# Kernel tuning notes

Measured on AMD Instinct MI355X. Metric: run time of the kernel, lower is better.

Reference implementation:

```python
import jax, jax.numpy as jnp
import numpy as np

DIM, SSM, RNN = 1024, 64, 128


def setup_inputs() -> dict:
    key = jax.random.key(0)
    ks = jax.random.split(key, 16)
    s = 0.02
    B, N = 8, 2048
    return {
        'x': jax.random.normal(ks[0], (B, N, DIM), jnp.float32),
        'A': jax.random.normal(ks[1], (SSM, SSM), jnp.float32) * s,
        'Bw': jax.random.normal(ks[2], (SSM, DIM), jnp.float32) * s,
        'Bb': jnp.zeros((SSM,), jnp.float32),
        'Cw': jax.random.normal(ks[3], (DIM, SSM), jnp.float32) * s,
        'Cb': jnp.zeros((DIM,), jnp.float32),
        'Dw': jax.random.normal(ks[4], (DIM, DIM), jnp.float32) * s,
        'Db': jnp.zeros((DIM,), jnp.float32),
        'W_ih': jax.random.normal(ks[5], (3 * RNN, DIM), jnp.float32) * s,
        'b_ih': jnp.zeros((3 * RNN,), jnp.float32),
        'W_hh': jax.random.normal(ks[6], (3 * RNN, RNN), jnp.float32) * s,
        'b_hh': jnp.zeros((3 * RNN,), jnp.float32),
        'proj_w': jax.random.normal(ks[7], (DIM, RNN), jnp.float32) * s,
        'proj_b': jnp.zeros((DIM,), jnp.float32),
        'gate_w': jax.random.normal(ks[8], (2, DIM), jnp.float32) * s,
        'gate_b': jnp.zeros((2,), jnp.float32),
    }


def reference(x, A, Bw, Bb, Cw, Cb, Dw, Db, W_ih, b_ih, W_hh, b_hh, proj_w, proj_b, gate_w, gate_b):
    B, N, D = x.shape
    R = W_hh.shape[1]
    # Precompute all input-side projections once (time-parallel GEMMs).
    bx = jnp.einsum('bnd,sd->bns', x, Bw) + Bb            # [B,N,SSM]
    dx = jnp.einsum('bnd,ed->bne', x, Dw) + Db            # [B,N,D]
    gx = jax.nn.sigmoid(jnp.einsum('bnd,gd->bng', x, gate_w) + gate_b)  # [B,N,2]
    ih = jnp.einsum('bnd,rd->bnr', x, W_ih) + b_ih        # [B,N,3R]
    # time-major for scan
    bx_t = jnp.swapaxes(bx, 0, 1)
    dx_t = jnp.swapaxes(dx, 0, 1)
    gx_t = jnp.swapaxes(gx, 0, 1)
    ih_t = jnp.swapaxes(ih, 0, 1)

    h_ssm0 = jnp.zeros((B, A.shape[0]), x.dtype)
    h_rnn0 = jnp.zeros((B, R), x.dtype)

    def step(carry, inp):
        h_ssm, h_rnn = carry
        bxt, dxt, gxt, iht = inp
        h_ssm = jax.nn.silu(h_ssm @ A.T + bxt)
        y_ssm = h_ssm @ Cw.T + Cb + dxt
        # GRUCell (torch semantics)
        hh = h_rnn @ W_hh.T + b_hh
        i_r, i_z, i_n = jnp.split(iht, 3, axis=-1)
        h_r, h_z, h_n = jnp.split(hh, 3, axis=-1)
        r = jax.nn.sigmoid(i_r + h_r)
        z = jax.nn.sigmoid(i_z + h_z)
        n = jnp.tanh(i_n + r * h_n)
        h_rnn = (1.0 - z) * n + z * h_rnn
        y_rnn = h_rnn @ proj_w.T + proj_b
        fused = gxt[:, :1] * y_ssm + gxt[:, 1:2] * y_rnn
        return (h_ssm, h_rnn), fused

    _, out = jax.lax.scan(step, (h_ssm0, h_rnn0), (bx_t, dx_t, gx_t, ih_t))
    return jnp.swapaxes(out, 0, 1)  # [B,N,D]
```

## Files before the change

kernel.cpp:

```cpp
#include <hip/hip_runtime.h>


#define MROWS 16384
#define SEQ   2048
#define CH    16
#define NCH   (SEQ / CH)

typedef __attribute__((ext_vector_type(8))) short bf16x8;
typedef __attribute__((ext_vector_type(4))) float f32x4;

__device__ __forceinline__ float bf2f(unsigned short u) {
    union { unsigned int i; float f; } c; c.i = ((unsigned int)u) << 16; return c.f;
}
__device__ __forceinline__ unsigned short f2bf(float f) {
    union { float f; unsigned int i; } c; c.f = f;
    unsigned int x = c.i;
    return (unsigned short)((x + 0x7fffu + ((x >> 16) & 1u)) >> 16);
}
__device__ __forceinline__ unsigned int f2bf_pk(float lo, float hi) {
    unsigned int r;
    asm("v_cvt_pk_bf16_f32 %0, %1, %2" : "=v"(r) : "v"(lo), "v"(hi));
    return r;
}
__device__ __forceinline__ float ldin(const void* p, size_t i, int isf32) {
    return isf32 ? ((const float*)p)[i] : bf2f(((const unsigned short*)p)[i]);
}
__device__ __forceinline__ float sigf(float v) { return 1.f / (1.f + __expf(-v)); }
__device__ __forceinline__ float tanhf_fast(float v) { return 2.f * sigf(2.f * v) - 1.f; }

__global__ void sniff_kernel(const unsigned short* __restrict__ x, int* __restrict__ flag) {
    int tid = threadIdx.x;
    int big = 0;
    for (int i = tid; i < 1024; i += 64) {
        unsigned int e = (x[i] >> 7) & 0xFFu;
        big += (e >= 0xC0u) ? 1 : 0;
    }
#pragma unroll
    for (int off = 32; off; off >>= 1) big += __shfl_down(big, off);
    if (tid == 0) { flag[0] = (big >= 4) ? 1 : 0; flag[1] = 0; }
}

__global__ void zero_out_kernel(float* __restrict__ out) {
    size_t i = ((size_t)blockIdx.x * 256 + threadIdx.x) * 16;
#pragma unroll
    for (int u = 0; u < 16; u++) out[i + u] = 0.f;
}

__device__ __forceinline__ void cvt16(const void* src, unsigned short* dst,
                                      size_t i0, int isf32) {
#pragma unroll
    for (int q = 0; q < 2; q++) {
        size_t i = i0 + q * 8;
        if (isf32) {
            const float* s = (const float*)src + i;
            float4 a = *reinterpret_cast<const float4*>(s);
            float4 b = *reinterpret_cast<const float4*>(s + 4);
            union { bf16x8 v; unsigned int u[4]; } u;
            u.u[0] = f2bf_pk(a.x, a.y); u.u[1] = f2bf_pk(a.z, a.w);
            u.u[2] = f2bf_pk(b.x, b.y); u.u[3] = f2bf_pk(b.z, b.w);
            *reinterpret_cast<bf16x8*>(dst + i) = u.v;
        } else {
            *reinterpret_cast<bf16x8*>(dst + i) =
                *reinterpret_cast<const bf16x8*>((const unsigned short*)src + i);
        }
    }
}

__global__ __launch_bounds__(256) void cvt_x_kernel(
    const void* __restrict__ x, unsigned short* __restrict__ xb,
    const int* __restrict__ flagp) {
    int isf32 = *flagp;
    size_t i0 = ((size_t)blockIdx.x * 256 + threadIdx.x) * 16;
    cvt16(x, xb, i0, isf32);
}

__global__ __launch_bounds__(256) void cvt_w_kernel(
    const void* __restrict__ Dw,  const void* __restrict__ Wih,
    const void* __restrict__ pw,  const void* __restrict__ Cw,
    const void* __restrict__ Bw,  const void* __restrict__ bih,
    const void* __restrict__ Bb,  const void* __restrict__ Cb,
    const void* __restrict__ Db,  const void* __restrict__ pb,
    unsigned short* __restrict__ Dwb,  unsigned short* __restrict__ Wihb,
    unsigned short* __restrict__ pwb,  unsigned short* __restrict__ Cwb,
    unsigned short* __restrict__ Bwb,  unsigned short* __restrict__ bihb,
    unsigned short* __restrict__ Bbb,  unsigned short* __restrict__ Cbb,
    unsigned short* __restrict__ Dbb,  unsigned short* __restrict__ pbb,
    const int* __restrict__ flagp) {
    int isf32 = *flagp;
    int blk = blockIdx.x, tid = threadIdx.x;
    const void* src; unsigned short* dst; size_t base;
    if (blk < 256)      { src = Dw;  dst = Dwb;  base = (size_t)blk * 4096; }
    else if (blk < 352) { src = Wih; dst = Wihb; base = (size_t)(blk - 256) * 4096; }
    else if (blk < 384) { src = pw;  dst = pwb;  base = (size_t)(blk - 352) * 4096; }
    else if (blk < 400) { src = Cw;  dst = Cwb;  base = (size_t)(blk - 384) * 4096; }
    else if (blk < 416) { src = Bw;  dst = Bwb;  base = (size_t)(blk - 400) * 4096; }
    else {
        for (int i = tid; i < 384; i += 256) bihb[i] = f2bf(ldin(bih, i, isf32));
        if (tid < 64) Bbb[tid] = f2bf(ldin(Bb, tid, isf32));
        for (int i = tid; i < 1024; i += 256) {
            Cbb[i] = f2bf(ldin(Cb, i, isf32));
            Dbb[i] = f2bf(ldin(Db, i, isf32));
            pbb[i] = f2bf(ldin(pb, i, isf32));
        }
        return;
    }
    cvt16(src, dst, base + (size_t)tid * 16, isf32);
}

__device__ __forceinline__ void stage_tile(const void* __restrict__ g,
                                           int ld, int row0, int rowmax, int kb,
                                           short (*lds)[40], int tid, int isf32) {
#pragma unroll
    for (int q = 0; q < 2; q++) {
        int oct = q * 256 + tid;
        int row = oct >> 2, c8 = (oct & 3) << 3;
        int gr = row0 + row; if (gr > rowmax) gr = rowmax;
        size_t base = (size_t)gr * ld + kb + c8;
        bf16x8 v;
        if (isf32) {
            const float* gp = (const float*)g + base;
            float4 f0 = *reinterpret_cast<const float4*>(gp);
            float4 f1 = *reinterpret_cast<const float4*>(gp + 4);
            union { bf16x8 v8; unsigned int u[4]; } u;
            u.u[0] = f2bf_pk(f0.x, f0.y);
            u.u[1] = f2bf_pk(f0.z, f0.w);
            u.u[2] = f2bf_pk(f1.x, f1.y);
            u.u[3] = f2bf_pk(f1.z, f1.w);
            v = u.v8;
        } else {
            v = *reinterpret_cast<const bf16x8*>((const unsigned short*)g + base);
        }
        *reinterpret_cast<bf16x8*>(&lds[row][c8]) = v;
    }
}

__device__ __forceinline__ void mfma_tiles(const short (*As)[40], const short (*Bs)[40],
                                           int wm, int wn, int lane, f32x4 (*acc)[4]) {
    bf16x8 af[4], bfr[4];
    int m = lane & 15, ko = (lane >> 4) << 3;
#pragma unroll
    for (int i = 0; i < 4; i++)
        af[i] = *reinterpret_cast<const bf16x8*>(&As[wm + i * 16 + m][ko]);
#pragma unroll
    for (int j = 0; j < 4; j++)
        bfr[j] = *reinterpret_cast<const bf16x8*>(&Bs[wn + j * 16 + m][ko]);
#pragma unroll
    for (int i = 0; i < 4; i++)
#pragma unroll
        for (int j = 0; j < 4; j++)
            acc[i][j] = __builtin_amdgcn_mfma_f32_16x16x32_bf16(af[i], bfr[j], acc[i][j], 0, 0, 0);
}

__global__ __launch_bounds__(256) void gemm_bt_kernel(
    const void* __restrict__ A, const void* __restrict__ W,
    const void* __restrict__ bias, unsigned short* __restrict__ C,
    int M, int N, int K, const int* __restrict__ flagp) {
    __shared__ __align__(16) short As[128][40];
    __shared__ __align__(16) short Bs[128][40];
    int isf32 = *flagp;
    int tid = threadIdx.x, lane = tid & 63, wave = tid >> 6;
    int wm = (wave >> 1) << 6, wn = (wave & 1) << 6;
    int tileM = blockIdx.x << 7, tileN = blockIdx.y << 7;
    f32x4 acc[4][4];
    f32x4 z = {0.f, 0.f, 0.f, 0.f};
#pragma unroll
    for (int i = 0; i < 4; i++)
#pragma unroll
        for (int j = 0; j < 4; j++) acc[i][j] = z;

    for (int kb = 0; kb < K; kb += 32) {
        __syncthreads();
        stage_tile(A, K, tileM, M - 1, kb, As, tid, isf32);
        stage_tile(W, K, tileN, N - 1, kb, Bs, tid, isf32);
        __syncthreads();
        mfma_tiles(As, Bs, wm, wn, lane, acc);
    }
#pragma unroll
    for (int i = 0; i < 4; i++) {
#pragma unroll
        for (int j = 0; j < 4; j++) {
            int col = tileN + wn + j * 16 + (lane & 15);
            if (col < N) {
                float bv = ldin(bias, col, isf32);
                int row0 = tileM + wm + i * 16 + ((lane >> 4) << 2);
                unsigned int pk0 = f2bf_pk(acc[i][j][0] + bv, acc[i][j][1] + bv);
                unsigned int pk1 = f2bf_pk(acc[i][j][2] + bv, acc[i][j][3] + bv);
                C[(size_t)(row0 + 0) * N + col] = (unsigned short)(pk0 & 0xFFFFu);
                C[(size_t)(row0 + 1) * N + col] = (unsigned short)(pk0 >> 16);
                C[(size_t)(row0 + 2) * N + col] = (unsigned short)(pk1 & 0xFFFFu);
                C[(size_t)(row0 + 3) * N + col] = (unsigned short)(pk1 >> 16);
            }
        }
    }
}

__global__ __launch_bounds__(256) void gate_kernel(
    const void* __restrict__ x, const void* __restrict__ gw,
    const void* __restrict__ gb, float* __restrict__ gx, const int* __restrict__ flagp) {
    int isf32 = *flagp;
    int row = (blockIdx.x << 2) + (threadIdx.x >> 6);
    int lane = threadIdx.x & 63;
    size_t xoff = (size_t)row * 1024 + lane * 16;
    float a0 = 0.f, a1 = 0.f;
#pragma unroll
    for (int q = 0; q < 2; q++) {
#pragma unroll
        for (int e = 0; e < 8; e++) {
            size_t k = q * 8 + e;
            float xf = ldin(x, xoff + k, isf32);
            a0 += xf * ldin(gw, (size_t)lane * 16 + k, isf32);
            a1 += xf * ldin(gw, 1024 + (size_t)lane * 16 + k, isf32);
        }
    }
#pragma unroll
    for (int off = 32; off > 0; off >>= 1) {
        a0 += __shfl_down(a0, off);
        a1 += __shfl_down(a1, off);
    }
    if (lane == 0) {
        gx[row * 2]     = sigf(a0 + ldin(gb, 0, isf32));
        gx[row * 2 + 1] = sigf(a1 + ldin(gb, 1, isf32));
    }
}

__global__ __launch_bounds__(512) void scan_kernel(
    const void* __restrict__ Amat,
    const void* __restrict__ Whh,
    const void* __restrict__ bhh,
    const unsigned short* __restrict__ bxw,
    const unsigned short* __restrict__ ihw,
    unsigned short* __restrict__ hsw,
    unsigned short* __restrict__ hrw,
    const int* __restrict__ flagp) {
    int isf32 = *flagp;
    int b = blockIdx.x & 7;
    size_t rowbase = (size_t)b * SEQ;
    f32x4 zf = {0.f, 0.f, 0.f, 0.f};

    if (blockIdx.x < 8) {
        __shared__ __align__(16) unsigned short H[2][128];
        __shared__ __align__(16) unsigned short IH[2][CH][384];
        int tid = threadIdx.x, lane = tid & 63, w = tid >> 6;
        int col = lane & 15, quad = lane >> 4;
        int o = w * 16 + col;
        if (tid < 256) ((unsigned short*)H)[tid] = 0;
        bf16x8 Bf[3][4];
#pragma unroll
        for (int g = 0; g < 3; g++) {
            int n = g * 128 + o;
#pragma unroll
            for (int c = 0; c < 4; c++) {
                int k0 = c * 32 + quad * 8;
                bf16x8 v;
#pragma unroll
                for (int e = 0; e < 8; e++)
                    v[e] = (short)f2bf(ldin(Whh, (size_t)n * 128 + k0 + e, isf32));
                Bf[g][c] = v;
            }
        }
        float bias_r = ldin(bhh, o, isf32);
        float bias_z = ldin(bhh, 128 + o, isf32);
        float bias_n = ldin(bhh, 256 + o, isf32);
        float hprev = 0.f;
        bool gl = (quad == 0);
        const unsigned short* ihbase = ihw + rowbase * 384;
        bf16x8 stg0, stg1;
        stg0 = *reinterpret_cast<const bf16x8*>(ihbase + (size_t)tid * 8);
        if (tid < 256) stg1 = *reinterpret_cast<const bf16x8*>(ihbase + (size_t)(512 + tid) * 8);
        *reinterpret_cast<bf16x8*>(&IH[0][0][0] + (size_t)tid * 8) = stg0;
        if (tid < 256) *reinterpret_cast<bf16x8*>(&IH[0][0][0] + (size_t)(512 + tid) * 8) = stg1;
        stg0 = *reinterpret_cast<const bf16x8*>(ihbase + (size_t)CH * 384 + (size_t)tid * 8);
        if (tid < 256) stg1 = *reinterpret_cast<const bf16x8*>(ihbase + (size_t)CH * 384 + (size_t)(512 + tid) * 8);
        __syncthreads();

        int p = 0;
        for (int c = 0; c < NCH; c++) {
            int cur = c & 1;
            for (int tt = 0; tt < CH; tt++) {
                int t = c * CH + tt;
                bf16x8 Af[4];
#pragma unroll
                for (int cc = 0; cc < 4; cc++)
                    Af[cc] = *reinterpret_cast<const bf16x8*>(&H[p][cc * 32 + quad * 8]);
                float ir  = bf2f(IH[cur][tt][o]);
                float iz  = bf2f(IH[cur][tt][128 + o]);
                float inn = bf2f(IH[cur][tt][256 + o]);
                f32x4 accL[3], accH[3];
#pragma unroll
                for (int g = 0; g < 3; g++) { accL[g] = zf; accH[g] = zf; }
                __builtin_amdgcn_s_setprio(1);
#pragma unroll
                for (int g = 0; g < 3; g++) {
                    accL[g] = __builtin_amdgcn_mfma_f32_16x16x32_bf16(Af[0], Bf[g][0], accL[g], 0, 0, 0);
                    accH[g] = __builtin_amdgcn_mfma_f32_16x16x32_bf16(Af[2], Bf[g][2], accH[g], 0, 0, 0);
                    accL[g] = __builtin_amdgcn_mfma_f32_16x16x32_bf16(Af[1], Bf[g][1], accL[g], 0, 0, 0);
                    accH[g] = __builtin_amdgcn_mfma_f32_16x16x32_bf16(Af[3], Bf[g][3], accH[g], 0, 0, 0);
                }
                __builtin_amdgcn_s_setprio(0);
                if (tt == 8) {
                    if (c + 1 < NCH) {
                        unsigned short* dst = &IH[(c + 1) & 1][0][0];
                        *reinterpret_cast<bf16x8*>(dst + (size_t)tid * 8) = stg0;
                        if (tid < 256) *reinterpret_cast<bf16x8*>(dst + (size_t)(512 + tid) * 8) = stg1;
                    }
                    if (c + 2 < NCH) {
                        const unsigned short* src = ihbase + (size_t)(c + 2) * CH * 384;
                        stg0 = *reinterpret_cast<const bf16x8*>(src + (size_t)tid * 8);
                        if (tid < 256) stg1 = *reinterpret_cast<const bf16x8*>(src + (size_t)(512 + tid) * 8);
                    }
                }
                float sr = accL[0][0] + accH[0][0];
                float sz = accL[1][0] + accH[1][0];
                float sn = accL[2][0] + accH[2][0];
                float r  = sigf(ir + sr + bias_r);
                float zg = sigf(iz + sz + bias_z);
                float n  = tanhf_fast(inn + r * (sn + bias_n));
                float hnew = (1.f - zg) * n + zg * hprev;
                hprev = hnew;
                if (gl) {
                    unsigned short hb = f2bf(hnew);
                    H[p ^ 1][o] = hb;
                    hrw[(rowbase + t) * 128 + o] = hb;
                }
                asm volatile("s_waitcnt lgkmcnt(0)" ::: "memory");
                __builtin_amdgcn_s_barrier();
                asm volatile("" ::: "memory");
                p ^= 1;
            }
        }
    } else {
        if (threadIdx.x >= 64) return;
        int lane = threadIdx.x, col = lane & 15, quad = lane >> 4;
        __shared__ __align__(16) unsigned short Hs[2][64];
        __shared__ __align__(16) unsigned short BX[2][CH][64];
        ((unsigned short*)Hs)[lane] = 0;
        ((unsigned short*)Hs)[64 + lane] = 0;
        bf16x8 Bf[4][2];
#pragma unroll
        for (int l = 0; l < 4; l++) {
            int n = l * 16 + col;
#pragma unroll
            for (int c = 0; c < 2; c++) {
                int k0 = c * 32 + quad * 8;
                bf16x8 v;
#pragma unroll
                for (int e = 0; e < 8; e++)
                    v[e] = (short)f2bf(ldin(Amat, (size_t)n * 64 + k0 + e, isf32));
                Bf[l][c] = v;
            }
        }
        bool gl = (quad == 0);
        const unsigned short* bxbase = bxw + rowbase * 64;
        bf16x8 stg[2];
#pragma unroll
        for (int q = 0; q < 2; q++)
            stg[q] = *reinterpret_cast<const bf16x8*>(bxbase + (size_t)(q * 64 + lane) * 8);
#pragma unroll
        for (int q = 0; q < 2; q++)
            *reinterpret_cast<bf16x8*>(&BX[0][0][0] + (size_t)(q * 64 + lane) * 8) = stg[q];
#pragma unroll
        for (int q = 0; q < 2; q++)
            stg[q] = *reinterpret_cast<const bf16x8*>(bxbase + (size_t)CH * 64 + (size_t)(q * 64 + lane) * 8);
        asm volatile("s_waitcnt lgkmcnt(0)" ::: "memory");

        int p = 0;
        for (int c = 0; c < NCH; c++) {
            int cur = c & 1;
            for (int tt = 0; tt < CH; tt++) {
                int t = c * CH + tt;
                bf16x8 Af[2];
#pragma unroll
                for (int cc = 0; cc < 2; cc++)
                    Af[cc] = *reinterpret_cast<const bf16x8*>(&Hs[p][cc * 32 + quad * 8]);
                float bx[4];
#pragma unroll
                for (int l = 0; l < 4; l++) bx[l] = bf2f(BX[cur][tt][l * 16 + col]);
                f32x4 acc[4];
#pragma unroll
                for (int l = 0; l < 4; l++) acc[l] = zf;
#pragma unroll
                for (int l = 0; l < 4; l++)
#pragma unroll
                    for (int cc = 0; cc < 2; cc++)
                        acc[l] = __builtin_amdgcn_mfma_f32_16x16x32_bf16(Af[cc], Bf[l][cc], acc[l], 0, 0, 0);
                if (tt == 8) {
                    if (c + 1 < NCH) {
                        unsigned short* dst = &BX[(c + 1) & 1][0][0];
#pragma unroll
                        for (int q = 0; q < 2; q++)
                            *reinterpret_cast<bf16x8*>(dst + (size_t)(q * 64 + lane) * 8) = stg[q];
                    }
                    if (c + 2 < NCH) {
#pragma unroll
                        for (int q = 0; q < 2; q++)
                            stg[q] = *reinterpret_cast<const bf16x8*>(
                                bxbase + (size_t)(c + 2) * CH * 64 + (size_t)(q * 64 + lane) * 8);
                    }
                }
#pragma unroll
                for (int l = 0; l < 4; l++) {
                    int o = l * 16 + col;
                    float v = acc[l][0] + bx[l];
                    float hv = v * sigf(v);
                    unsigned short hb = f2bf(hv);
                    if (gl) {
                        Hs[p ^ 1][o] = hb;
                        hsw[(rowbase + t) * 64 + o] = hb;
                    }
                }
                asm volatile("s_waitcnt lgkmcnt(0)" ::: "memory");
                p ^= 1;
            }
        }
    }
}

__global__ __launch_bounds__(256) void out_kernel(
    const void* __restrict__ x,  const void* __restrict__ Dw, const void* __restrict__ Db,
    const unsigned short* __restrict__ hs, const void* __restrict__ Cw, const void* __restrict__ Cb,
    const unsigned short* __restrict__ hr, const void* __restrict__ pw, const void* __restrict__ pb,
    const float* __restrict__ gx, float* __restrict__ out,
    const int* __restrict__ flagp) {
    __shared__ __align__(16) short As[128][40];
    __shared__ __align__(16) short Bs[128][40];
    int isf32 = *flagp;
    int tid = threadIdx.x, lane = tid & 63, wave = tid >> 6;
    int wm = (wave >> 1) << 6, wn = (wave & 1) << 6;
    int tileM = blockIdx.x << 7, tileN = blockIdx.y << 7;
    f32x4 z = {0.f, 0.f, 0.f, 0.f};
    f32x4 acc1[4][4], acc2[4][4];
#pragma unroll
    for (int i = 0; i < 4; i++)
#pragma unroll
        for (int j = 0; j < 4; j++) { acc1[i][j] = z; acc2[i][j] = z; }

    for (int kb = 0; kb < 1024; kb += 32) {
        __syncthreads();
        stage_tile(x,  1024, tileM, MROWS - 1, kb, As, tid, isf32);
        stage_tile(Dw, 1024, tileN, 1023, kb, Bs, tid, isf32);
        __syncthreads();
        mfma_tiles(As, Bs, wm, wn, lane, acc1);
    }
    for (int kb = 0; kb < 64; kb += 32) {
        __syncthreads();
        stage_tile(hs, 64, tileM, MROWS - 1, kb, As, tid, 0);
        stage_tile(Cw, 64, tileN, 1023, kb, Bs, tid, isf32);
        __syncthreads();
        mfma_tiles(As, Bs, wm, wn, lane, acc1);
    }
    for (int kb = 0; kb < 128; kb += 32) {
        __syncthreads();
        stage_tile(hr, 128, tileM, MROWS - 1, kb, As, tid, 0);
        stage_tile(pw, 128, tileN, 1023, kb, Bs, tid, isf32);
        __syncthreads();
        mfma_tiles(As, Bs, wm, wn, lane, acc2);
    }
#pragma unroll
    for (int i = 0; i < 4; i++) {
        int r0 = tileM + wm + i * 16 + ((lane >> 4) << 2);
#pragma unroll
        for (int j = 0; j < 4; j++) {
            int col = tileN + wn + j * 16 + (lane & 15);
            float cb  = ldin(Cb, col, isf32) + ldin(Db, col, isf32);
            float pbv = ldin(pb, col, isf32);
#pragma unroll
            for (int r = 0; r < 4; r++) {
                int row = r0 + r;
                float g0 = gx[row * 2], g1 = gx[row * 2 + 1];
                out[(size_t)row * 1024 + col] =
                    g0 * (acc1[i][j][r] + cb) + g1 * (acc2[i][j][r] + pbv);
            }
        }
    }
}

extern "C" void kernel_launch(void* const* d_in, const int* in_sizes, int n_in,
                              void* d_out, int out_size, void* d_ws, size_t ws_size,
                              hipStream_t stream) {
    static const int expect_sizes[16] = {16777216, 4096, 65536, 64, 65536, 1024,
                                         1048576, 1024, 393216, 384, 49152, 384,
                                         131072, 1024, 2048, 2};
    bool order_ok = (n_in == 16);
    if (order_ok)
        for (int i = 0; i < 16; i++)
            if (in_sizes[i] != expect_sizes[i]) { order_ok = false; break; }
    float* out = (float*)d_out;
    if (!order_ok) {
        zero_out_kernel<<<dim3(4096), dim3(256), 0, stream>>>(out);
        return;
    }

    const void* x    = d_in[0];
    const void* Amat = d_in[1];
    const void* Bw   = d_in[2];
    const void* Bb   = d_in[3];
    const void* Cw   = d_in[4];
    const void* Cb   = d_in[5];
    const void* Dw   = d_in[6];
    const void* Db   = d_in[7];
    const void* Wih  = d_in[8];
    const void* bih  = d_in[9];
    const void* Whh  = d_in[10];
    const void* bhh  = d_in[11];
    const void* pw   = d_in[12];
    const void* pb   = d_in[13];
    const void* gw   = d_in[14];
    const void* gb   = d_in[15];

    char* ws = (char*)d_ws;
    int*            flg = (int*)(ws);
    float*          gxw = (float*)(ws + 256);
    unsigned short* hsw = (unsigned short*)(ws + 131328);
    unsigned short* hrw = (unsigned short*)(ws + 2228480);
    unsigned short* bxw = (unsigned short*)(ws + 6422784);
    unsigned short* ihw = (unsigned short*)(ws + 8519936);
    unsigned short* xb   = (unsigned short*)(ws + 21102848);
    unsigned short* Dwb  = (unsigned short*)(ws + 54657280);
    unsigned short* Wihb = (unsigned short*)(ws + 56754432);
    unsigned short* pwb  = (unsigned short*)(ws + 57540864);
    unsigned short* Cwb  = (unsigned short*)(ws + 57803008);
    unsigned short* Bwb  = (unsigned short*)(ws + 57934080);
    unsigned short* bihb = (unsigned short*)(ws + 58065152);
    unsigned short* Bbb  = (unsigned short*)(ws + 58069248);
    unsigned short* Cbb  = (unsigned short*)(ws + 58073344);
    unsigned short* Dbb  = (unsigned short*)(ws + 58077440);
    unsigned short* pbb  = (unsigned short*)(ws + 58081536);
    bool big = ws_size >= 58085632ull;

    dim3 blk(256);
    sniff_kernel<<<dim3(1), dim3(64), 0, stream>>>((const unsigned short*)x, flg);
    if (big) {
        cvt_x_kernel<<<dim3(4096), blk, 0, stream>>>(x, xb, flg);
        cvt_w_kernel<<<dim3(417), blk, 0, stream>>>(
            Dw, Wih, pw, Cw, Bw, bih, Bb, Cb, Db, pb,
            Dwb, Wihb, pwb, Cwb, Bwb, bihb, Bbb, Cbb, Dbb, pbb, flg);
        gemm_bt_kernel<<<dim3(128, 3), blk, 0, stream>>>(xb, Wihb, bihb, ihw, MROWS, 384, 1024, flg + 1);
        gemm_bt_kernel<<<dim3(128, 1), blk, 0, stream>>>(xb, Bwb, Bbb, bxw, MROWS, 64, 1024, flg + 1);
        gate_kernel<<<dim3(4096), blk, 0, stream>>>(x, gw, gb, gxw, flg);
        scan_kernel<<<dim3(16), dim3(512), 0, stream>>>(Amat, Whh, bhh, bxw, ihw, hsw, hrw, flg);
        out_kernel<<<dim3(128, 8), blk, 0, stream>>>(xb, Dwb, Dbb, hsw, Cwb, Cbb, hrw, pwb, pbb, gxw, out, flg + 1);
    } else {
        gemm_bt_kernel<<<dim3(128, 3), blk, 0, stream>>>(x, Wih, bih, ihw, MROWS, 384, 1024, flg);
        gemm_bt_kernel<<<dim3(128, 1), blk, 0, stream>>>(x, Bw, Bb, bxw, MROWS, 64, 1024, flg);
        gate_kernel<<<dim3(4096), blk, 0, stream>>>(x, gw, gb, gxw, flg);
        scan_kernel<<<dim3(16), dim3(512), 0, stream>>>(Amat, Whh, bhh, bxw, ihw, hsw, hrw, flg);
        out_kernel<<<dim3(128, 8), blk, 0, stream>>>(x, Dw, Db, hsw, Cw, Cb, hrw, pw, pb, gxw, out, flg);
    }
}
```

Baseline: 1.447 ms.

## Merge conversion, GEMM and gate kernels; overlap gate work with scan

Folds the x and weight conversion kernels into one launch, and merges the two input-projection GEMMs into one grid that picks weights per blockIdx.y. The gate projection now runs as extra blocks of the scan kernel, so it uses otherwise idle CUs while the 16 serial scan blocks run. The scan loops are split around the staging point, which removes the per-step tt==8 branch and the setprio calls. This cuts launch overhead and hides the gate pass behind the latency-bound scan, at the cost of a 512-thread block size for gate work and possible contention with the scan blocks.

```diff
diff --git a/kernel.cpp b/kernel.cpp
--- a/kernel.cpp
+++ b/kernel.cpp
@@ -66,20 +66,14 @@
     }
 }
 
-__global__ __launch_bounds__(256) void cvt_x_kernel(
-    const void* __restrict__ x, unsigned short* __restrict__ xb,
-    const int* __restrict__ flagp) {
-    int isf32 = *flagp;
-    size_t i0 = ((size_t)blockIdx.x * 256 + threadIdx.x) * 16;
-    cvt16(x, xb, i0, isf32);
-}
-
-__global__ __launch_bounds__(256) void cvt_w_kernel(
+__global__ __launch_bounds__(256) void cvt_all_kernel(
+    const void* __restrict__ x,
     const void* __restrict__ Dw,  const void* __restrict__ Wih,
     const void* __restrict__ pw,  const void* __restrict__ Cw,
     const void* __restrict__ Bw,  const void* __restrict__ bih,
     const void* __restrict__ Bb,  const void* __restrict__ Cb,
     const void* __restrict__ Db,  const void* __restrict__ pb,
+    unsigned short* __restrict__ xb,
     unsigned short* __restrict__ Dwb,  unsigned short* __restrict__ Wihb,
     unsigned short* __restrict__ pwb,  unsigned short* __restrict__ Cwb,
     unsigned short* __restrict__ Bwb,  unsigned short* __restrict__ bihb,
@@ -87,7 +81,13 @@
     unsigned short* __restrict__ Dbb,  unsigned short* __restrict__ pbb,
     const int* __restrict__ flagp) {
     int isf32 = *flagp;
-    int blk = blockIdx.x, tid = threadIdx.x;
+    int tid = threadIdx.x;
+    if (blockIdx.x < 4096) {
+        size_t i0 = ((size_t)blockIdx.x * 256 + tid) * 16;
+        cvt16(x, xb, i0, isf32);
+        return;
+    }
+    int blk = blockIdx.x - 4096;
     const void* src; unsigned short* dst; size_t base;
     if (blk < 256)      { src = Dw;  dst = Dwb;  base = (size_t)blk * 4096; }
     else if (blk < 352) { src = Wih; dst = Wihb; base = (size_t)(blk - 256) * 4096; }
@@ -151,16 +151,20 @@
             acc[i][j] = __builtin_amdgcn_mfma_f32_16x16x32_bf16(af[i], bfr[j], acc[i][j], 0, 0, 0);
 }
 
-__global__ __launch_bounds__(256) void gemm_bt_kernel(
-    const void* __restrict__ A, const void* __restrict__ W,
-    const void* __restrict__ bias, unsigned short* __restrict__ C,
-    int M, int N, int K, const int* __restrict__ flagp) {
+__global__ __launch_bounds__(256) void gemm_fused_kernel(
+    const void* __restrict__ A,
+    const void* __restrict__ Wih, const void* __restrict__ bih, unsigned short* __restrict__ C1,
+    const void* __restrict__ Bw,  const void* __restrict__ Bb,  unsigned short* __restrict__ C2,
+    const int* __restrict__ flagp) {
     __shared__ __align__(16) short As[128][40];
     __shared__ __align__(16) short Bs[128][40];
     int isf32 = *flagp;
     int tid = threadIdx.x, lane = tid & 63, wave = tid >> 6;
     int wm = (wave >> 1) << 6, wn = (wave & 1) << 6;
-    int tileM = blockIdx.x << 7, tileN = blockIdx.y << 7;
+    int tileM = blockIdx.x << 7;
+    const void* W; const void* bias; unsigned short* C; int N, tileN;
+    if (blockIdx.y < 3) { W = Wih; bias = bih; C = C1; N = 384; tileN = blockIdx.y << 7; }
+    else                { W = Bw;  bias = Bb;  C = C2; N = 64;  tileN = 0; }
     f32x4 acc[4][4];
     f32x4 z = {0.f, 0.f, 0.f, 0.f};
 #pragma unroll
@@ -168,10 +172,10 @@
 #pragma unroll
         for (int j = 0; j < 4; j++) acc[i][j] = z;
 
-    for (int kb = 0; kb < K; kb += 32) {
-        __syncthreads();
-        stage_tile(A, K, tileM, M - 1, kb, As, tid, isf32);
-        stage_tile(W, K, tileN, N - 1, kb, Bs, tid, isf32);
+    for (int kb = 0; kb < 1024; kb += 32) {
+        __syncthreads();
+        stage_tile(A, 1024, tileM, MROWS - 1, kb, As, tid, isf32);
+        stage_tile(W, 1024, tileN, N - 1, kb, Bs, tid, isf32);
         __syncthreads();
         mfma_tiles(As, Bs, wm, wn, lane, acc);
     }
@@ -194,35 +198,6 @@
     }
 }
 
-__global__ __launch_bounds__(256) void gate_kernel(
-    const void* __restrict__ x, const void* __restrict__ gw,
-    const void* __restrict__ gb, float* __restrict__ gx, const int* __restrict__ flagp) {
-    int isf32 = *flagp;
-    int row = (blockIdx.x << 2) + (threadIdx.x >> 6);
-    int lane = threadIdx.x & 63;
-    size_t xoff = (size_t)row * 1024 + lane * 16;
-    float a0 = 0.f, a1 = 0.f;
-#pragma unroll
-    for (int q = 0; q < 2; q++) {
-#pragma unroll
-        for (int e = 0; e < 8; e++) {
-            size_t k = q * 8 + e;
-            float xf = ldin(x, xoff + k, isf32);
-            a0 += xf * ldin(gw, (size_t)lane * 16 + k, isf32);
-            a1 += xf * ldin(gw, 1024 + (size_t)lane * 16 + k, isf32);
-        }
-    }
-#pragma unroll
-    for (int off = 32; off > 0; off >>= 1) {
-        a0 += __shfl_down(a0, off);
-        a1 += __shfl_down(a1, off);
-    }
-    if (lane == 0) {
-        gx[row * 2]     = sigf(a0 + ldin(gb, 0, isf32));
-        gx[row * 2 + 1] = sigf(a1 + ldin(gb, 1, isf32));
-    }
-}
-
 __global__ __launch_bounds__(512) void scan_kernel(
     const void* __restrict__ Amat,
     const void* __restrict__ Whh,
@@ -231,11 +206,41 @@
     const unsigned short* __restrict__ ihw,
     unsigned short* __restrict__ hsw,
     unsigned short* __restrict__ hrw,
+    const void* __restrict__ x,  const void* __restrict__ gw,
+    const void* __restrict__ gb, float* __restrict__ gx,
     const int* __restrict__ flagp) {
     int isf32 = *flagp;
+    f32x4 zf = {0.f, 0.f, 0.f, 0.f};
+
+    if (blockIdx.x >= 16) {
+        int row = (int)(blockIdx.x - 16) * 8 + (threadIdx.x >> 6);
+        int lane = threadIdx.x & 63;
+        size_t xoff = (size_t)row * 1024 + lane * 16;
+        float a0 = 0.f, a1 = 0.f;
+#pragma unroll
+        for (int q = 0; q < 2; q++) {
+#pragma unroll
+            for (int e = 0; e < 8; e++) {
+                size_t k = q * 8 + e;
+                float xf = ldin(x, xoff + k, isf32);
+                a0 += xf * ldin(gw, (size_t)lane * 16 + k, isf32);
+                a1 += xf * ldin(gw, 1024 + (size_t)lane * 16 + k, isf32);
+            }
+        }
+#pragma unroll
+        for (int off = 32; off > 0; off >>= 1) {
+            a0 += __shfl_down(a0, off);
+            a1 += __shfl_down(a1, off);
+        }
+        if (lane == 0) {
+            gx[row * 2]     = sigf(a0 + ldin(gb, 0, isf32));
+            gx[row * 2 + 1] = sigf(a1 + ldin(gb, 1, isf32));
+        }
+        return;
+    }
+
     int b = blockIdx.x & 7;
     size_t rowbase = (size_t)b * SEQ;
-    f32x4 zf = {0.f, 0.f, 0.f, 0.f};
 
     if (blockIdx.x < 8) {
         __shared__ __align__(16) unsigned short H[2][128];
@@ -274,59 +279,55 @@
         __syncthreads();
 
         int p = 0;
+        auto gru_step = [&](int t, int cur, int tt) {
+            bf16x8 Af[4];
+#pragma unroll
+            for (int cc = 0; cc < 4; cc++)
+                Af[cc] = *reinterpret_cast<const bf16x8*>(&H[p][cc * 32 + quad * 8]);
+            float ir  = bf2f(IH[cur][tt][o]);
+            float iz  = bf2f(IH[cur][tt][128 + o]);
+            float inn = bf2f(IH[cur][tt][256 + o]);
+            f32x4 aL[3], aH[3];
+#pragma unroll
+            for (int g = 0; g < 3; g++) {
+                aL[g] = __builtin_amdgcn_mfma_f32_16x16x32_bf16(Af[0], Bf[g][0], zf, 0, 0, 0);
+                aH[g] = __builtin_amdgcn_mfma_f32_16x16x32_bf16(Af[2], Bf[g][2], zf, 0, 0, 0);
+                aL[g] = __builtin_amdgcn_mfma_f32_16x16x32_bf16(Af[1], Bf[g][1], aL[g], 0, 0, 0);
+                aH[g] = __builtin_amdgcn_mfma_f32_16x16x32_bf16(Af[3], Bf[g][3], aH[g], 0, 0, 0);
+            }
+            float sr = aL[0][0] + aH[0][0];
+            float sz = aL[1][0] + aH[1][0];
+            float sn = aL[2][0] + aH[2][0];
+            float r  = sigf(ir + sr + bias_r);
+            float zg = sigf(iz + sz + bias_z);
+            float n  = tanhf_fast(inn + r * (sn + bias_n));
+            float hnew = (1.f - zg) * n + zg * hprev;
+            hprev = hnew;
+            if (gl) {
+                unsigned short hb = f2bf(hnew);
+                H[p ^ 1][o] = hb;
+                hrw[(rowbase + t) * 128 + o] = hb;
+            }
+            asm volatile("s_waitcnt lgkmcnt(0)" ::: "memory");
+            __builtin_amdgcn_s_barrier();
+            asm volatile("" ::: "memory");
+            p ^= 1;
+        };
+
         for (int c = 0; c < NCH; c++) {
             int cur = c & 1;
-            for (int tt = 0; tt < CH; tt++) {
-                int t = c * CH + tt;
-                bf16x8 Af[4];
-#pragma unroll
-                for (int cc = 0; cc < 4; cc++)
-                    Af[cc] = *reinterpret_cast<const bf16x8*>(&H[p][cc * 32 + quad * 8]);
-                float ir  = bf2f(IH[cur][tt][o]);
-                float iz  = bf2f(IH[cur][tt][128 + o]);
-                float inn = bf2f(IH[cur][tt][256 + o]);
-                f32x4 accL[3], accH[3];
-#pragma unroll
-                for (int g = 0; g < 3; g++) { accL[g] = zf; accH[g] = zf; }
-                __builtin_amdgcn_s_setprio(1);
-#pragma unroll
-                for (int g = 0; g < 3; g++) {
-                    accL[g] = __builtin_amdgcn_mfma_f32_16x16x32_bf16(Af[0], Bf[g][0], accL[g], 0, 0, 0);
-                    accH[g] = __builtin_amdgcn_mfma_f32_16x16x32_bf16(Af[2], Bf[g][2], accH[g], 0, 0, 0);
-                    accL[g] = __builtin_amdgcn_mfma_f32_16x16x32_bf16(Af[1], Bf[g][1], accL[g], 0, 0, 0);
-                    accH[g] = __builtin_amdgcn_mfma_f32_16x16x32_bf16(Af[3], Bf[g][3], accH[g], 0, 0, 0);
+            for (int tt = 0; tt < 8; tt++) gru_step(c * CH + tt, cur, tt);
+            if (c + 1 < NCH) {
+                unsigned short* dst = &IH[(c + 1) & 1][0][0];
+                *reinterpret_cast<bf16x8*>(dst + (size_t)tid * 8) = stg0;
+                if (tid < 256) *reinterpret_cast<bf16x8*>(dst + (size_t)(512 + tid) * 8) = stg1;
+                if (c + 2 < NCH) {
+                    const unsigned short* src = ihbase + (size_t)(c + 2) * CH * 384;
+                    stg0 = *reinterpret_cast<const bf16x8*>(src + (size_t)tid * 8);
+                    if (tid < 256) stg1 = *reinterpret_cast<const bf16x8*>(src + (size_t)(512 + tid) * 8);
                 }
-                __builtin_amdgcn_s_setprio(0);
-                if (tt == 8) {
-                    if (c + 1 < NCH) {
-                        unsigned short* dst = &IH[(c + 1) & 1][0][0];
-                        *reinterpret_cast<bf16x8*>(dst + (size_t)tid * 8) = stg0;
-                        if (tid < 256) *reinterpret_cast<bf16x8*>(dst + (size_t)(512 + tid) * 8) = stg1;
-                    }
-                    if (c + 2 < NCH) {
-                        const unsigned short* src = ihbase + (size_t)(c + 2) * CH * 384;
-                        stg0 = *reinterpret_cast<const bf16x8*>(src + (size_t)tid * 8);
-                        if (tid < 256) stg1 = *reinterpret_cast<const bf16x8*>(src + (size_t)(512 + tid) * 8);
-                    }
-                }
-                float sr = accL[0][0] + accH[0][0];
-                float sz = accL[1][0] + accH[1][0];
-                float sn = accL[2][0] + accH[2][0];
-                float r  = sigf(ir + sr + bias_r);
-                float zg = sigf(iz + sz + bias_z);
-                float n  = tanhf_fast(inn + r * (sn + bias_n));
-                float hnew = (1.f - zg) * n + zg * hprev;
-                hprev = hnew;
-                if (gl) {
-                    unsigned short hb = f2bf(hnew);
-                    H[p ^ 1][o] = hb;
-                    hrw[(rowbase + t) * 128 + o] = hb;
-                }
-                asm volatile("s_waitcnt lgkmcnt(0)" ::: "memory");
-                __builtin_amdgcn_s_barrier();
-                asm volatile("" ::: "memory");
-                p ^= 1;
-            }
+            }
+            for (int tt = 8; tt < CH; tt++) gru_step(c * CH + tt, cur, tt);
         }
     } else {
         if (threadIdx.x >= 64) return;
@@ -364,53 +365,51 @@
         asm volatile("s_waitcnt lgkmcnt(0)" ::: "memory");
 
         int p = 0;
+        auto ssm_step = [&](int t, int cur, int tt) {
+            bf16x8 Af[2];
+#pragma unroll
+            for (int cc = 0; cc < 2; cc++)
+                Af[cc] = *reinterpret_cast<const bf16x8*>(&Hs[p][cc * 32 + quad * 8]);
+            float bx[4];
+#pragma unroll
+            for (int l = 0; l < 4; l++) bx[l] = bf2f(BX[cur][tt][l * 16 + col]);
+            f32x4 acc[4];
+#pragma unroll
+            for (int l = 0; l < 4; l++) {
+                acc[l] = __builtin_amdgcn_mfma_f32_16x16x32_bf16(Af[0], Bf[l][0], zf, 0, 0, 0);
+                acc[l] = __builtin_amdgcn_mfma_f32_16x16x32_bf16(Af[1], Bf[l][1], acc[l], 0, 0, 0);
+            }
+#pragma unroll
+            for (int l = 0; l < 4; l++) {
+                int o = l * 16 + col;
+                float v = acc[l][0] + bx[l];
+                float hv = v * sigf(v);
+                unsigned short hb = f2bf(hv);
+                if (gl) {
+                    Hs[p ^ 1][o] = hb;
+                    hsw[(rowbase + t) * 64 + o] = hb;
+                }
+            }
+            asm volatile("s_waitcnt lgkmcnt(0)" ::: "memory");
+            p ^= 1;
+        };
+
         for (int c = 0; c < NCH; c++) {
             int cur = c & 1;
-            for (int tt = 0; tt < CH; tt++) {
-                int t = c * CH + tt;
-                bf16x8 Af[2];
-#pragma unroll
-                for (int cc = 0; cc < 2; cc++)
-                    Af[cc] = *reinterpret_cast<const bf16x8*>(&Hs[p][cc * 32 + quad * 8]);
-                float bx[4];
-#pragma unroll
-                for (int l = 0; l < 4; l++) bx[l] = bf2f(BX[cur][tt][l * 16 + col]);
-                f32x4 acc[4];
-#pragma unroll
-                for (int l = 0; l < 4; l++) acc[l] = zf;
-#pragma unroll
-                for (int l = 0; l < 4; l++)
-#pragma unroll
-                    for (int cc = 0; cc < 2; cc++)
-                        acc[l] = __builtin_amdgcn_mfma_f32_16x16x32_bf16(Af[cc], Bf[l][cc], acc[l], 0, 0, 0);
-                if (tt == 8) {
-                    if (c + 1 < NCH) {
-                        unsigned short* dst = &BX[(c + 1) & 1][0][0];
-#pragma unroll
-                        for (int q = 0; q < 2; q++)
-                            *reinterpret_cast<bf16x8*>(dst + (size_t)(q * 64 + lane) * 8) = stg[q];
-                    }
-                    if (c + 2 < NCH) {
-#pragma unroll
-                        for (int q = 0; q < 2; q++)
-                            stg[q] = *reinterpret_cast<const bf16x8*>(
-                                bxbase + (size_t)(c + 2) * CH * 64 + (size_t)(q * 64 + lane) * 8);
-                    }
+            for (int tt = 0; tt < 8; tt++) ssm_step(c * CH + tt, cur, tt);
+            if (c + 1 < NCH) {
+                unsigned short* dst = &BX[(c + 1) & 1][0][0];
+#pragma unroll
+                for (int q = 0; q < 2; q++)
+                    *reinterpret_cast<bf16x8*>(dst + (size_t)(q * 64 + lane) * 8) = stg[q];
+                if (c + 2 < NCH) {
+#pragma unroll
+                    for (int q = 0; q < 2; q++)
+                        stg[q] = *reinterpret_cast<const bf16x8*>(
+                            bxbase + (size_t)(c + 2) * CH * 64 + (size_t)(q * 64 + lane) * 8);
                 }
-#pragma unroll
-                for (int l = 0; l < 4; l++) {
-                    int o = l * 16 + col;
-                    float v = acc[l][0] + bx[l];
-                    float hv = v * sigf(v);
-                    unsigned short hb = f2bf(hv);
-                    if (gl) {
-                        Hs[p ^ 1][o] = hb;
-                        hsw[(rowbase + t) * 64 + o] = hb;
-                    }
-                }
-                asm volatile("s_waitcnt lgkmcnt(0)" ::: "memory");
-                p ^= 1;
-            }
+            }
+            for (int tt = 8; tt < CH; tt++) ssm_step(c * CH + tt, cur, tt);
         }
     }
 }
@@ -530,20 +529,21 @@
     dim3 blk(256);
     sniff_kernel<<<dim3(1), dim3(64), 0, stream>>>((const unsigned short*)x, flg);
     if (big) {
-        cvt_x_kernel<<<dim3(4096), blk, 0, stream>>>(x, xb, flg);
-        cvt_w_kernel<<<dim3(417), blk, 0, stream>>>(
-            Dw, Wih, pw, Cw, Bw, bih, Bb, Cb, Db, pb,
-            Dwb, Wihb, pwb, Cwb, Bwb, bihb, Bbb, Cbb, Dbb, pbb, flg);
-        gemm_bt_kernel<<<dim3(128, 3), blk, 0, stream>>>(xb, Wihb, bihb, ihw, MROWS, 384, 1024, flg + 1);
-        gemm_bt_kernel<<<dim3(128, 1), blk, 0, stream>>>(xb, Bwb, Bbb, bxw, MROWS, 64, 1024, flg + 1);
-        gate_kernel<<<dim3(4096), blk, 0, stream>>>(x, gw, gb, gxw, flg);
-        scan_kernel<<<dim3(16), dim3(512), 0, stream>>>(Amat, Whh, bhh, bxw, ihw, hsw, hrw, flg);
-        out_kernel<<<dim3(128, 8), blk, 0, stream>>>(xb, Dwb, Dbb, hsw, Cwb, Cbb, hrw, pwb, pbb, gxw, out, flg + 1);
+        cvt_all_kernel<<<dim3(4513), blk, 0, stream>>>(
+            x, Dw, Wih, pw, Cw, Bw, bih, Bb, Cb, Db, pb,
+            xb, Dwb, Wihb, pwb, Cwb, Bwb, bihb, Bbb, Cbb, Dbb, pbb, flg);
+        gemm_fused_kernel<<<dim3(128, 4), blk, 0, stream>>>(
+            xb, Wihb, bihb, ihw, Bwb, Bbb, bxw, flg + 1);
+        scan_kernel<<<dim3(2064), dim3(512), 0, stream>>>(
+            Amat, Whh, bhh, bxw, ihw, hsw, hrw, x, gw, gb, gxw, flg);
+        out_kernel<<<dim3(128, 8), blk, 0, stream>>>(
+            xb, Dwb, Dbb, hsw, Cwb, Cbb, hrw, pwb, pbb, gxw, out, flg + 1);
     } else {
-        gemm_bt_kernel<<<dim3(128, 3), blk, 0, stream>>>(x, Wih, bih, ihw, MROWS, 384, 1024, flg);
-        gemm_bt_kernel<<<dim3(128, 1), blk, 0, stream>>>(x, Bw, Bb, bxw, MROWS, 64, 1024, flg);
-        gate_kernel<<<dim3(4096), blk, 0, stream>>>(x, gw, gb, gxw, flg);
-        scan_kernel<<<dim3(16), dim3(512), 0, stream>>>(Amat, Whh, bhh, bxw, ihw, hsw, hrw, flg);
-        out_kernel<<<dim3(128, 8), blk, 0, stream>>>(x, Dw, Db, hsw, Cw, Cb, hrw, pw, pb, gxw, out, flg);
-    }
-}
+        gemm_fused_kernel<<<dim3(128, 4), blk, 0, stream>>>(
+            x, Wih, bih, ihw, Bw, Bb, bxw, flg);
+        scan_kernel<<<dim3(2064), dim3(512), 0, stream>>>(
+            Amat, Whh, bhh, bxw, ihw, hsw, hrw, x, gw, gb, gxw, flg);
+        out_kernel<<<dim3(128, 8), blk, 0, stream>>>(
+            x, Dw, Db, hsw, Cw, Cb, hrw, pw, pb, gxw, out, flg);
+    }
+}
```

Result: faster. 1.303 ms (-9.9%).
